# Optimization experiments

Hardware: AMD Instinct MI355X
Metric: run time of the kernel (lower is better)

Reference implementation:

```python
import jax, jax.numpy as jnp
import numpy as np

# hyperparameters (from init_kwargs)
GAMMA = 2.0
KEEP_WEIGHT = 1.0
T_TEMP = 0.07
M = 0.5
COS_M = float(np.cos(M))
SIN_M = float(np.sin(M))
THRESHOLD = float(np.cos(np.pi - M))
MM = float(np.sin(np.pi - M) * M)
ALPHA = 0.1
T_BUF0 = 0.0  # registered buffer t initialized to zero
VALID_THRESHOLD = 0.8
EPS = 1e-12  # F.normalize eps


def setup_inputs() -> dict:
    key = jax.random.key(0)
    k1, k2, k3 = jax.random.split(key, 3)
    N, C = 8192, 128
    return {
        "feature1": jax.random.normal(k1, (N, C), jnp.float32),
        "feature2": jax.random.normal(k2, (N, C), jnp.float32),
        "labels": jax.random.randint(k3, (N,), 0, 1024, dtype=jnp.int32),
    }


def reference(feature1, feature2, labels):
    N = feature1.shape[0]
    f1 = feature1 / jnp.maximum(jnp.linalg.norm(feature1, axis=1, keepdims=True), EPS)
    f2 = feature2 / jnp.maximum(jnp.linalg.norm(feature2, axis=1, keepdims=True), EPS)

    # [N, N] similarity, clamped to [-1, 1]
    sim = jnp.clip(jnp.einsum('nc,kc->nk', f1, f2), -1.0, 1.0)

    pos = (labels[:, None] == labels[None, :]).astype(sim.dtype)  # [N, N]
    neg = 1.0 - pos
    pos_mask = pos > 0

    # buffer update t (no_grad in original)
    mean_ts = jax.lax.stop_gradient((sim * pos).sum() / pos.sum())
    t = ALPHA * mean_ts + (1.0 - ALPHA) * T_BUF0
    weight_valid = t > VALID_THRESHOLD

    # curricular margin on positive entries
    sin_theta = jnp.sqrt(1.0 - sim * sim)
    cos_theta_m = sim * COS_M - sin_theta * SIN_M
    final_pos = jnp.where(sim > THRESHOLD, cos_theta_m, sim - MM)
    sim2 = jnp.where(pos_mask, final_pos, sim)

    # per-row mean of (margined) positive similarities
    row_target = (sim2 * pos).sum(axis=1) / pos.sum(axis=1)  # [N]
    hard_mask = sim2 > row_target[:, None]
    sim3 = jnp.where(hard_mask, sim2 * (t + sim2), sim2)
    sim4 = jnp.where(pos_mask, final_pos, sim3)

    logits = jnp.exp(sim4 / T_TEMP)

    # focal-style reweighting (only used when weight_valid)
    diff_pos = (pos - sim * pos) ** GAMMA + KEEP_WEIGHT * pos
    diff_neg = jnp.clip(sim * neg, 0.0, 1.0) ** GAMMA + KEEP_WEIGHT * neg

    logit_pos = jnp.where(weight_valid, (logits * diff_pos).sum(axis=1), (logits * pos).sum(axis=1))
    logit_neg = jnp.where(weight_valid, (logits * diff_neg).sum(axis=1), (logits * neg).sum(axis=1))

    loss = -jnp.log(logit_pos / (logit_neg + logit_pos)).sum() / N
    return loss
```

## Files before the change

### kernel.cpp

```cpp
#include <hip/hip_runtime.h>

#define N_ROWS 8192
#define N_LBL  1024
#define KMAX   64

constexpr float C_COS_M  = (float)0.8775825618903728;
constexpr float C_SIN_M  = (float)0.479425538604203;
constexpr float C_THRESH = (float)-0.8775825618903728;
constexpr float C_MM     = (float)0.2397127693021015;
constexpr float C_ALPHA  = 0.1f;
constexpr float C_VALID  = 0.8f;
constexpr float C_K2E    = (float)(1.0 / (0.07 * 0.6931471805599453));
constexpr float C_LN2    = 0.6931471805599453f;

typedef short s16x8 __attribute__((ext_vector_type(8)));
typedef float f32x4 __attribute__((ext_vector_type(4)));

__device__ __forceinline__ unsigned f2bf(float f) {
    unsigned u = __float_as_uint(f);
    return (u + 0x7fffu + ((u >> 16) & 1u)) >> 16;
}
__device__ __forceinline__ float bflo(unsigned u) { return __uint_as_float(u << 16); }
__device__ __forceinline__ float bfhi(unsigned u) { return __uint_as_float(u & 0xffff0000u); }

__device__ __forceinline__ void gl_lds16(const unsigned* g, void* lds) {
    __builtin_amdgcn_global_load_lds(
        (const __attribute__((address_space(1))) unsigned*)g,
        (__attribute__((address_space(3))) unsigned*)lds, 16, 0, 0);
}

__global__ void k_norm(const float* __restrict__ f1, const float* __restrict__ f2,
                       const int* __restrict__ labels,
                       unsigned* __restrict__ f1n, unsigned* __restrict__ f2n,
                       int* __restrict__ hist, unsigned short* __restrict__ bucket,
                       float* __restrict__ out) {
    if (blockIdx.x == 0 && threadIdx.x == 0) out[0] = 0.f;
    int b = blockIdx.x * 4 + (threadIdx.x >> 6);
    int l = threadIdx.x & 63;
    int row = (b < N_ROWS) ? b : (b - N_ROWS);
    const float* src = (b < N_ROWS) ? f1 : f2;
    unsigned* dst = (b < N_ROWS) ? f1n : f2n;
    float2 v = ((const float2*)(src + row * 128))[l];
    float ss = v.x * v.x + v.y * v.y;
    #pragma unroll
    for (int k = 1; k < 64; k <<= 1) ss += __shfl_xor(ss, k);
    float inv = 1.0f / fmaxf(sqrtf(ss), 1e-12f);
    dst[row * 64 + l] = f2bf(v.x * inv) | (f2bf(v.y * inv) << 16);
    if (b < N_ROWS && l == 0) {
        int lab = labels[row];
        int p = atomicAdd(&hist[lab], 1);
        if (p < KMAX) bucket[lab * KMAX + p] = (unsigned short)row;
    }
}

__global__ __launch_bounds__(64) void k_passA(const unsigned* __restrict__ f1n,
                                              const unsigned* __restrict__ f2n,
                                              const int* __restrict__ labels,
                                              const int* __restrict__ hist,
                                              const unsigned short* __restrict__ bucket,
                                              float* __restrict__ rt,
                                              float* __restrict__ row_sim,
                                              int* __restrict__ rowcnt,
                                              float* __restrict__ simlist) {
    int i = blockIdx.x, lane = threadIdx.x;
    int g = lane >> 4, sl = lane & 15;
    uint4 a = ((const uint4*)(f1n + i * 64))[sl];
    float a0 = bflo(a.x), a1 = bfhi(a.x), a2 = bflo(a.y), a3 = bfhi(a.y);
    float a4 = bflo(a.z), a5 = bfhi(a.z), a6 = bflo(a.w), a7 = bfhi(a.w);
    int lab = labels[i];
    int cnt = hist[lab];
    int cntc = cnt < KMAX ? cnt : KMAX;
    float rs_sim = 0.f, rs_fp = 0.f;
    for (int e0 = 0; e0 < cntc; e0 += 4) {
        int e = e0 + g;
        bool val = e < cntc;
        int j = bucket[lab * KMAX + (val ? e : 0)];
        uint4 b = ((const uint4*)(f2n + j * 64))[sl];
        float p = a0 * bflo(b.x) + a1 * bfhi(b.x) + a2 * bflo(b.y) + a3 * bfhi(b.y)
                + a4 * bflo(b.z) + a5 * bfhi(b.z) + a6 * bflo(b.w) + a7 * bfhi(b.w);
        p += __shfl_xor(p, 1);
        p += __shfl_xor(p, 2);
        p += __shfl_xor(p, 4);
        p += __shfl_xor(p, 8);
        float s = fminf(1.f, fmaxf(-1.f, p));
        float ctm = s * C_COS_M - sqrtf(fmaxf(0.f, 1.f - s * s)) * C_SIN_M;
        float fpv = (s > C_THRESH) ? ctm : (s - C_MM);
        if (val) {
            rs_sim += s;
            rs_fp += fpv;
            if (sl == 0) simlist[i * KMAX + e] = s;
        }
    }
    rs_sim += __shfl_xor(rs_sim, 16); rs_sim += __shfl_xor(rs_sim, 32);
    rs_fp  += __shfl_xor(rs_fp, 16);  rs_fp  += __shfl_xor(rs_fp, 32);
    if (lane == 0) {
        rt[i] = rs_fp / (float)cnt;
        row_sim[i] = rs_sim;
        rowcnt[i] = cnt;
    }
}

__global__ void k_finalize(const float* __restrict__ row_sim, const int* __restrict__ hist,
                           float* __restrict__ tw) {
    int t = threadIdx.x;
    float ssum = 0.f, scnt = 0.f;
    if (t < N_LBL) { float h = (float)hist[t]; scnt = h * h; }
    #pragma unroll
    for (int p = 0; p < 8; ++p) ssum += row_sim[p * 1024 + t];
    #pragma unroll
    for (int k = 1; k < 64; k <<= 1) {
        ssum += __shfl_xor(ssum, k);
        scnt += __shfl_xor(scnt, k);
    }
    __shared__ float sa[16], sb[16];
    if ((t & 63) == 0) { sa[t >> 6] = ssum; sb[t >> 6] = scnt; }
    __syncthreads();
    if (t == 0) {
        float s1 = 0.f, s2 = 0.f;
        #pragma unroll
        for (int w = 0; w < 16; ++w) { s1 += sa[w]; s2 += sb[w]; }
        tw[0] = C_ALPHA * s1 / s2;
    }
}

__global__ __launch_bounds__(256, 3) void k_passB(const unsigned* __restrict__ f1n,
                                                  const unsigned* __restrict__ f2n,
                                                  const float* __restrict__ rt,
                                                  const float* __restrict__ tw,
                                                  float* __restrict__ lnacc2) {
    __shared__ __align__(16) unsigned char ldsA[32768];
    const int tid = threadIdx.x;
    const int wave = tid >> 6, lane = tid & 63;
    const int wr = wave >> 1, wc = wave & 1;
    const int quad = lane >> 4, l15 = lane & 15;
    const int rowbase = blockIdx.x * 128;
    const float tval = tw[0];
    const bool wv = (tval > C_VALID);

    {
        const int srow = tid >> 4;
        const int sq   = (tid & 15) ^ (srow & 15);
        const unsigned* gA = f1n + rowbase * 64 + srow * 64 + sq * 4;
        const int loff = wave * 1024;
        #pragma unroll
        for (int it = 0; it < 8; ++it)
            gl_lds16(gA + it * 1024, ldsA + loff + it * 4096);
    }

    float rtv[4][4];
    #pragma unroll
    for (int mt = 0; mt < 4; ++mt)
        #pragma unroll
        for (int r = 0; r < 4; ++r)
            rtv[mt][r] = rt[rowbase + wr * 64 + mt * 16 + quad * 4 + r];

    __syncthreads();

    s16x8 af[4][4];
    #pragma unroll
    for (int mt = 0; mt < 4; ++mt)
        #pragma unroll
        for (int ks = 0; ks < 4; ++ks) {
            int row = wr * 64 + mt * 16 + l15, q = ks * 4 + quad;
            af[mt][ks] = *((const s16x8*)(ldsA + row * 256 + ((q ^ (row & 15)) << 4)));
        }

    const unsigned* bb = f2n + (blockIdx.y * 1024 + wc * 512 + l15) * 64 + quad * 4;

    float lnp[4][4] = {};

    auto loadB = [&](s16x8* b, int ct) {
        const unsigned* p = bb + ct * 1024;
        #pragma unroll
        for (int ks = 0; ks < 4; ++ks)
            b[ks] = *((const s16x8*)(p + ks * 16));
    };
    auto tile = [&](const s16x8* b) {
        f32x4 acc[4];
        #pragma unroll
        for (int mt = 0; mt < 4; ++mt) acc[mt] = (f32x4){0.f, 0.f, 0.f, 0.f};
        #pragma unroll
        for (int ks = 0; ks < 4; ++ks)
            #pragma unroll
            for (int mt = 0; mt < 4; ++mt)
                acc[mt] = __builtin_amdgcn_mfma_f32_16x16x32_bf16(af[mt][ks], b[ks],
                                                                  acc[mt], 0, 0, 0);
        #pragma unroll
        for (int mt = 0; mt < 4; ++mt)
            #pragma unroll
            for (int r = 0; r < 4; ++r) {
                float s = acc[mt][r];
                float u = C_K2E * s;
                float m = tval + s;
                float arg = (s > rtv[mt][r]) ? u * m : u;
                float e = __builtin_amdgcn_exp2f(arg);
                if (wv) { float cz = fmaxf(s, 0.f); e = e * (cz * cz + 1.f); }
                lnp[mt][r] += e;
            }
    };

    s16x8 b0[4], b1[4];
    loadB(b0, 0);
    #pragma unroll 1
    for (int ct = 0; ct < 32; ct += 2) {
        loadB(b1, ct + 1);
        tile(b0);
        if (ct + 2 < 32) loadB(b0, ct + 2);
        tile(b1);
    }

    const int slice = blockIdx.y * 2 + wc;
    #pragma unroll
    for (int mt = 0; mt < 4; ++mt)
        #pragma unroll
        for (int r = 0; r < 4; ++r) {
            float v = lnp[mt][r];
            v += __shfl_xor(v, 1);
            v += __shfl_xor(v, 2);
            v += __shfl_xor(v, 4);
            v += __shfl_xor(v, 8);
            if (l15 == 0)
                lnacc2[slice * N_ROWS + rowbase + wr * 64 + mt * 16 + quad * 4 + r] = v;
        }
}

__global__ void k_lossC(const float* __restrict__ simlist, const int* __restrict__ rowcnt,
                        const float* __restrict__ rt, const float* __restrict__ tw,
                        const float* __restrict__ lnacc2, float* __restrict__ out) {
    int t = threadIdx.x;
    int sub = t >> 3, sl = t & 7;
    int i = blockIdx.x * 32 + sub;
    int cnt = rowcnt[i];
    if (cnt > KMAX) cnt = KMAX;
    float tval = tw[0];
    bool wv = (tval > C_VALID);
    float rti = rt[i];
    float lp = 0.f, den = 0.f;
    for (int e = sl; e < cnt; e += 8) {
        float s = simlist[i * KMAX + e];
        float sh = (s > rti) ? s * (tval + s) : s;
        float en = __builtin_amdgcn_exp2f(C_K2E * sh);
        float ctm = s * C_COS_M - sqrtf(fmaxf(0.f, 1.f - s * s)) * C_SIN_M;
        float fp = (s > C_THRESH) ? ctm : (s - C_MM);
        float ep = __builtin_amdgcn_exp2f(C_K2E * fp);
        if (wv) {
            float cz = fmaxf(s, 0.f);
            en *= cz * cz + 1.f;
            float d = 1.f - s;
            ep *= d * d + 1.f;
        }
        den -= en;
        lp += ep;
    }
    float lnsum = 0.f;
    #pragma unroll
    for (int p = 0; p < 2; ++p) lnsum += lnacc2[(sl + p * 8) * N_ROWS + i];
    #pragma unroll
    for (int k = 1; k < 8; k <<= 1) {
        den += __shfl_xor(den, k);
        lp += __shfl_xor(lp, k);
        lnsum += __shfl_xor(lnsum, k);
    }
    float ln = lnsum + den;
    float rl = (__builtin_amdgcn_logf(lp + ln) - __builtin_amdgcn_logf(lp)) * C_LN2;
    rl += __shfl_xor(rl, 8);
    rl += __shfl_xor(rl, 16);
    rl += __shfl_xor(rl, 32);
    __shared__ float sa[4];
    if ((t & 63) == 0) sa[t >> 6] = rl;
    __syncthreads();
    if (t == 0)
        atomicAdd(out, (sa[0] + sa[1] + sa[2] + sa[3]) * (1.0f / (float)N_ROWS));
}

extern "C" void kernel_launch(void* const* d_in, const int* in_sizes, int n_in,
                              void* d_out, int out_size, void* d_ws, size_t ws_size,
                              hipStream_t stream) {
    (void)in_sizes; (void)n_in; (void)out_size; (void)ws_size;
    const float* f1 = (const float*)d_in[0];
    const float* f2 = (const float*)d_in[1];
    const int* labels = (const int*)d_in[2];
    float* out = (float*)d_out;
    char* ws = (char*)d_ws;

    unsigned* f1n          = (unsigned*)(ws + 0);
    unsigned* f2n          = (unsigned*)(ws + 2097152);
    float* simlist         = (float*)(ws + 4194304);
    float* rt              = (float*)(ws + 6291456);
    float* row_sim         = (float*)(ws + 6324224);
    int* rowcnt            = (int*)(ws + 6356992);
    float* lnacc2          = (float*)(ws + 6389760);
    unsigned short* bucket = (unsigned short*)(ws + 6914048);
    float* tw              = (float*)(ws + 7045120);
    int* hist              = (int*)(ws + 7045184);

    hipMemsetAsync(hist, 0, 4096, stream);

    k_norm<<<dim3(4096), dim3(256), 0, stream>>>(f1, f2, labels, f1n, f2n, hist, bucket, out);
    k_passA<<<dim3(N_ROWS), dim3(64), 0, stream>>>(f1n, f2n, labels, hist, bucket,
                                                   rt, row_sim, rowcnt, simlist);
    k_finalize<<<dim3(1), dim3(1024), 0, stream>>>(row_sim, hist, tw);
    k_passB<<<dim3(64, 8), dim3(256), 0, stream>>>(f1n, f2n, rt, tw, lnacc2);
    k_lossC<<<dim3(256), dim3(256), 0, stream>>>(simlist, rowcnt, rt, tw, lnacc2, out);
}
```

Measured before the change: 118.6 us.

## Fuse finalize into passA via last-block reduction and retile passB to 512 threads

k_finalize is removed and folded into k_passA: each block now handles four rows, and the last block to finish (found with an atomic done counter) reduces row_sim and hist to compute t, saving one kernel launch. k_passB moves to 512-thread blocks with 8 waves covering 32 rows each and half as many columns per block, doubling the grid's y dimension and the lnacc2 slices that k_lossC sums. The weight_valid branch is hoisted out of the inner loop with compile-time template dispatch. The trade-offs are an extra atomic and fence in passA and more partial-sum slices to read in k_lossC.

```diff
diff --git a/kernel.cpp b/kernel.cpp
--- a/kernel.cpp
+++ b/kernel.cpp
@@ -15,6 +15,9 @@
 
 typedef short s16x8 __attribute__((ext_vector_type(8)));
 typedef float f32x4 __attribute__((ext_vector_type(4)));
+
+struct WvTrue  { static constexpr bool value = true;  };
+struct WvFalse { static constexpr bool value = false; };
 
 __device__ __forceinline__ unsigned f2bf(float f) {
     unsigned u = __float_as_uint(f);
@@ -53,16 +56,20 @@
     }
 }
 
-__global__ __launch_bounds__(64) void k_passA(const unsigned* __restrict__ f1n,
-                                              const unsigned* __restrict__ f2n,
-                                              const int* __restrict__ labels,
-                                              const int* __restrict__ hist,
-                                              const unsigned short* __restrict__ bucket,
-                                              float* __restrict__ rt,
-                                              float* __restrict__ row_sim,
-                                              int* __restrict__ rowcnt,
-                                              float* __restrict__ simlist) {
-    int i = blockIdx.x, lane = threadIdx.x;
+__global__ __launch_bounds__(256) void k_passA(const unsigned* __restrict__ f1n,
+                                               const unsigned* __restrict__ f2n,
+                                               const int* __restrict__ labels,
+                                               const int* __restrict__ hist,
+                                               const unsigned short* __restrict__ bucket,
+                                               float* __restrict__ rt,
+                                               float* __restrict__ row_sim,
+                                               int* __restrict__ rowcnt,
+                                               float* __restrict__ simlist,
+                                               int* __restrict__ done,
+                                               float* __restrict__ tw) {
+    int tid = threadIdx.x;
+    int lane = tid & 63;
+    int i = blockIdx.x * 4 + (tid >> 6);
     int g = lane >> 4, sl = lane & 15;
     uint4 a = ((const uint4*)(f1n + i * 64))[sl];
     float a0 = bflo(a.x), a1 = bfhi(a.x), a2 = bflo(a.y), a3 = bfhi(a.y);
@@ -98,32 +105,35 @@
         row_sim[i] = rs_sim;
         rowcnt[i] = cnt;
     }
-}
-
-__global__ void k_finalize(const float* __restrict__ row_sim, const int* __restrict__ hist,
-                           float* __restrict__ tw) {
-    int t = threadIdx.x;
-    float ssum = 0.f, scnt = 0.f;
-    if (t < N_LBL) { float h = (float)hist[t]; scnt = h * h; }
-    #pragma unroll
-    for (int p = 0; p < 8; ++p) ssum += row_sim[p * 1024 + t];
+    __threadfence();
+    __syncthreads();
+    __shared__ int lastFlag;
+    if (tid == 0) lastFlag = (atomicAdd(done, 1) == (int)gridDim.x - 1);
+    __syncthreads();
+    if (!lastFlag) return;
+    __threadfence();
+    float s1 = 0.f;
+    #pragma unroll
+    for (int k = 0; k < 32; ++k) s1 += row_sim[tid + 256 * k];
+    float s2 = 0.f;
+    #pragma unroll
+    for (int k = 0; k < 4; ++k) { float h = (float)hist[tid + 256 * k]; s2 += h * h; }
     #pragma unroll
     for (int k = 1; k < 64; k <<= 1) {
-        ssum += __shfl_xor(ssum, k);
-        scnt += __shfl_xor(scnt, k);
-    }
-    __shared__ float sa[16], sb[16];
-    if ((t & 63) == 0) { sa[t >> 6] = ssum; sb[t >> 6] = scnt; }
-    __syncthreads();
-    if (t == 0) {
-        float s1 = 0.f, s2 = 0.f;
-        #pragma unroll
-        for (int w = 0; w < 16; ++w) { s1 += sa[w]; s2 += sb[w]; }
-        tw[0] = C_ALPHA * s1 / s2;
-    }
-}
-
-__global__ __launch_bounds__(256, 3) void k_passB(const unsigned* __restrict__ f1n,
+        s1 += __shfl_xor(s1, k);
+        s2 += __shfl_xor(s2, k);
+    }
+    __shared__ float sa[4], sb[4];
+    if (lane == 0) { sa[tid >> 6] = s1; sb[tid >> 6] = s2; }
+    __syncthreads();
+    if (tid == 0) {
+        float num = sa[0] + sa[1] + sa[2] + sa[3];
+        float den = sb[0] + sb[1] + sb[2] + sb[3];
+        tw[0] = C_ALPHA * num / den;
+    }
+}
+
+__global__ __launch_bounds__(512, 4) void k_passB(const unsigned* __restrict__ f1n,
                                                   const unsigned* __restrict__ f2n,
                                                   const float* __restrict__ rt,
                                                   const float* __restrict__ tw,
@@ -143,31 +153,31 @@
         const unsigned* gA = f1n + rowbase * 64 + srow * 64 + sq * 4;
         const int loff = wave * 1024;
         #pragma unroll
-        for (int it = 0; it < 8; ++it)
-            gl_lds16(gA + it * 1024, ldsA + loff + it * 4096);
-    }
-
-    float rtv[4][4];
-    #pragma unroll
-    for (int mt = 0; mt < 4; ++mt)
+        for (int it = 0; it < 4; ++it)
+            gl_lds16(gA + it * 2048, ldsA + loff + it * 8192);
+    }
+
+    float rtv[2][4];
+    #pragma unroll
+    for (int mt = 0; mt < 2; ++mt)
         #pragma unroll
         for (int r = 0; r < 4; ++r)
-            rtv[mt][r] = rt[rowbase + wr * 64 + mt * 16 + quad * 4 + r];
-
-    __syncthreads();
-
-    s16x8 af[4][4];
-    #pragma unroll
-    for (int mt = 0; mt < 4; ++mt)
+            rtv[mt][r] = rt[rowbase + wr * 32 + mt * 16 + quad * 4 + r];
+
+    __syncthreads();
+
+    s16x8 af[2][4];
+    #pragma unroll
+    for (int mt = 0; mt < 2; ++mt)
         #pragma unroll
         for (int ks = 0; ks < 4; ++ks) {
-            int row = wr * 64 + mt * 16 + l15, q = ks * 4 + quad;
+            int row = wr * 32 + mt * 16 + l15, q = ks * 4 + quad;
             af[mt][ks] = *((const s16x8*)(ldsA + row * 256 + ((q ^ (row & 15)) << 4)));
         }
 
-    const unsigned* bb = f2n + (blockIdx.y * 1024 + wc * 512 + l15) * 64 + quad * 4;
-
-    float lnp[4][4] = {};
+    const unsigned* bb = f2n + (blockIdx.y * 512 + wc * 256 + l15) * 64 + quad * 4;
+
+    float lnp[2][4] = {};
 
     auto loadB = [&](s16x8* b, int ct) {
         const unsigned* p = bb + ct * 1024;
@@ -175,43 +185,48 @@
         for (int ks = 0; ks < 4; ++ks)
             b[ks] = *((const s16x8*)(p + ks * 16));
     };
-    auto tile = [&](const s16x8* b) {
-        f32x4 acc[4];
-        #pragma unroll
-        for (int mt = 0; mt < 4; ++mt) acc[mt] = (f32x4){0.f, 0.f, 0.f, 0.f};
+    auto tile = [&](const s16x8* b, auto wvc) {
+        f32x4 acc[2];
+        #pragma unroll
+        for (int mt = 0; mt < 2; ++mt) acc[mt] = (f32x4){0.f, 0.f, 0.f, 0.f};
         #pragma unroll
         for (int ks = 0; ks < 4; ++ks)
             #pragma unroll
-            for (int mt = 0; mt < 4; ++mt)
+            for (int mt = 0; mt < 2; ++mt)
                 acc[mt] = __builtin_amdgcn_mfma_f32_16x16x32_bf16(af[mt][ks], b[ks],
                                                                   acc[mt], 0, 0, 0);
         #pragma unroll
-        for (int mt = 0; mt < 4; ++mt)
+        for (int mt = 0; mt < 2; ++mt)
             #pragma unroll
             for (int r = 0; r < 4; ++r) {
                 float s = acc[mt][r];
                 float u = C_K2E * s;
-                float m = tval + s;
-                float arg = (s > rtv[mt][r]) ? u * m : u;
+                float arg = (s > rtv[mt][r]) ? u * (tval + s) : u;
                 float e = __builtin_amdgcn_exp2f(arg);
-                if (wv) { float cz = fmaxf(s, 0.f); e = e * (cz * cz + 1.f); }
+                if constexpr (decltype(wvc)::value) {
+                    float cz = fmaxf(s, 0.f);
+                    e = e * (cz * cz + 1.f);
+                }
                 lnp[mt][r] += e;
             }
     };
 
-    s16x8 b0[4], b1[4];
-    loadB(b0, 0);
-    #pragma unroll 1
-    for (int ct = 0; ct < 32; ct += 2) {
-        loadB(b1, ct + 1);
-        tile(b0);
-        if (ct + 2 < 32) loadB(b0, ct + 2);
-        tile(b1);
-    }
+    auto run = [&](auto wvc) {
+        s16x8 b0[4], b1[4];
+        loadB(b0, 0);
+        #pragma unroll 1
+        for (int ct = 0; ct < 16; ct += 2) {
+            loadB(b1, ct + 1);
+            tile(b0, wvc);
+            if (ct + 2 < 16) loadB(b0, ct + 2);
+            tile(b1, wvc);
+        }
+    };
+    if (wv) run(WvTrue{}); else run(WvFalse{});
 
     const int slice = blockIdx.y * 2 + wc;
     #pragma unroll
-    for (int mt = 0; mt < 4; ++mt)
+    for (int mt = 0; mt < 2; ++mt)
         #pragma unroll
         for (int r = 0; r < 4; ++r) {
             float v = lnp[mt][r];
@@ -220,7 +235,7 @@
             v += __shfl_xor(v, 4);
             v += __shfl_xor(v, 8);
             if (l15 == 0)
-                lnacc2[slice * N_ROWS + rowbase + wr * 64 + mt * 16 + quad * 4 + r] = v;
+                lnacc2[slice * N_ROWS + rowbase + wr * 32 + mt * 16 + quad * 4 + r] = v;
         }
 }
 
@@ -254,7 +269,7 @@
     }
     float lnsum = 0.f;
     #pragma unroll
-    for (int p = 0; p < 2; ++p) lnsum += lnacc2[(sl + p * 8) * N_ROWS + i];
+    for (int p = 0; p < 4; ++p) lnsum += lnacc2[(sl + p * 8) * N_ROWS + i];
     #pragma unroll
     for (int k = 1; k < 8; k <<= 1) {
         den += __shfl_xor(den, k);
@@ -290,16 +305,16 @@
     float* row_sim         = (float*)(ws + 6324224);
     int* rowcnt            = (int*)(ws + 6356992);
     float* lnacc2          = (float*)(ws + 6389760);
-    unsigned short* bucket = (unsigned short*)(ws + 6914048);
-    float* tw              = (float*)(ws + 7045120);
-    int* hist              = (int*)(ws + 7045184);
-
-    hipMemsetAsync(hist, 0, 4096, stream);
+    unsigned short* bucket = (unsigned short*)(ws + 7438336);
+    float* tw              = (float*)(ws + 7569408);
+    int* hist              = (int*)(ws + 7569472);
+    int* done              = (int*)(ws + 7573568);
+
+    hipMemsetAsync(hist, 0, 4100, stream);
 
     k_norm<<<dim3(4096), dim3(256), 0, stream>>>(f1, f2, labels, f1n, f2n, hist, bucket, out);
-    k_passA<<<dim3(N_ROWS), dim3(64), 0, stream>>>(f1n, f2n, labels, hist, bucket,
-                                                   rt, row_sim, rowcnt, simlist);
-    k_finalize<<<dim3(1), dim3(1024), 0, stream>>>(row_sim, hist, tw);
-    k_passB<<<dim3(64, 8), dim3(256), 0, stream>>>(f1n, f2n, rt, tw, lnacc2);
+    k_passA<<<dim3(2048), dim3(256), 0, stream>>>(f1n, f2n, labels, hist, bucket,
+                                                  rt, row_sim, rowcnt, simlist, done, tw);
+    k_passB<<<dim3(64, 16), dim3(512), 0, stream>>>(f1n, f2n, rt, tw, lnacc2);
     k_lossC<<<dim3(256), dim3(256), 0, stream>>>(simlist, rowcnt, rt, tw, lnacc2, out);
 }
```

New measurement: 306.1 us. +158.0%, slower.
